# Performance work log

Measured on AMD Instinct MI355X. Metric: run time of the kernel, lower is better.

Reference implementation:

```python
import jax, jax.numpy as jnp
import numpy as np

THRESHOLD = 0.5
MARGIN = 0.5
MIN_PIXELS = 64


def make_grid(h, w):
    # Faithful to SpatialClustering.make_grid
    if w >= h:
        xm = jnp.broadcast_to(jnp.linspace(0.0, w / h, w).reshape(1, 1, w), (1, h, w))
        ym = jnp.broadcast_to(jnp.linspace(0.0, 1.0, h).reshape(1, h, 1), (1, h, w))
    else:
        xm = jnp.broadcast_to(jnp.linspace(0.0, 1.0, w).reshape(1, 1, w), (1, h, w))
        ym = jnp.broadcast_to(jnp.linspace(0.0, h / w, h).reshape(1, h, 1), (1, h, w))
    return jnp.concatenate([xm, ym], axis=0)  # (2, h, w)


def cluster_per_image(x, grid_flat):
    # x: (5, h, w); grid_flat: (2, N)
    c, h, w = x.shape
    N = h * w
    offset = x[0:2].reshape(2, N)
    sigma = x[2:4].reshape(2, N)
    seed_raw = x[4].reshape(N)

    spa_emb = jnp.tanh(offset) + grid_flat          # (2, N)
    seed_map = jax.nn.sigmoid(seed_raw)             # (N,)
    valid = seed_raw > THRESHOLD                    # (N,) == torch `mask`

    # In torch: masked_select restricts to `valid` pixels; here we keep the
    # full N-length arrays and carry `valid`/`unclustered` boolean masks.
    # unclustered starts as `valid`, so the torch outer guard
    # (mask.sum() > min_pixels) coincides with the first while-cond check.

    def cond(state):
        unclustered, inst, count, done = state
        return (jnp.sum(unclustered) > MIN_PIXELS) & jnp.logical_not(done)

    def body(state):
        unclustered, inst, count, done = state
        score = jnp.where(unclustered, seed_map, 0.0)
        idx = jnp.argmax(score)
        sc = score[idx]
        new_done = sc < THRESHOLD  # torch `break` -> revert this iteration's updates

        uncl2 = unclustered.at[idx].set(False)  # torch: unclustered[seed] = 0 before ratio
        center = spa_emb[:, idx]                # (2,)
        s = sigma[:, idx]                       # (2,)
        # exp(-sum((e-c)^2 / (2 s^2)))
        dist = jnp.exp(-jnp.sum((spa_emb - center[:, None]) ** 2 / (2.0 * s[:, None] ** 2), axis=0))  # (N,)
        proposal = (dist > MARGIN) & valid

        pc = jnp.sum(proposal)
        uc = jnp.sum(proposal & uncl2)
        # torch: proposal.sum() > min_pixels  and  unclustered[proposal].sum()/proposal.sum() > 0.5
        accept = (pc > MIN_PIXELS) & (2 * uc > pc)

        inst_new = jnp.where(accept & proposal, count, inst)
        count_new = count + accept.astype(jnp.int32)
        uncl_new = uncl2 & jnp.logical_not(proposal)  # torch: unclustered[proposal] = 0

        unclustered = jnp.where(new_done, unclustered, uncl_new)
        inst = jnp.where(new_done, inst, inst_new)
        count = jnp.where(new_done, count, count_new)
        return (unclustered, inst, count, new_done)

    init = (valid, jnp.zeros(N, dtype=jnp.int32), jnp.int32(1), jnp.array(False))
    _, inst, _, _ = jax.lax.while_loop(cond, body, init)
    return inst.reshape(h, w)


def setup_inputs() -> dict:
    key = jax.random.key(0)
    k1, k2, k3 = jax.random.split(key, 3)
    B, H, W = 4, 512, 1024
    offset = jax.random.normal(k1, (B, 2, H, W), dtype=jnp.float32)
    # sigma in [0.2, 0.45]: realistic per-pixel bandwidths so exp-distance
    # proposals cover cluster-sized regions and the greedy loop terminates.
    sigma = jax.random.uniform(k2, (B, 2, H, W), dtype=jnp.float32, minval=0.2, maxval=0.45)
    seed = jax.random.normal(k3, (B, 1, H, W), dtype=jnp.float32)
    tag_pred = jnp.concatenate([offset, sigma, seed], axis=1)  # (B, 5, H, W)
    return {"tag_pred": tag_pred}


def reference(tag_pred):
    b, c, h, w = tag_pred.shape
    grid_flat = make_grid(h, w).reshape(2, h * w)
    f = lambda x: cluster_per_image(x, grid_flat)
    inst = jax.lax.map(f, tag_pred)  # sequential per-image greedy clustering
    return inst.astype(jnp.uint8)    # (b, h, w) instance map, ids 0 = background
```

## Files before the change

### kernel.cpp

```cpp
#include <hip/hip_runtime.h>
#include <math.h>

#define BATCH 4
#define HH 512
#define WW 1024
#define NPIX (HH*WW)
#define CCAP 196608
#define GX 64
#define GY 48
#define NCELL (GX*GY)
#define CELL 0.0625f
#define INVCELL 16.0f
#define SEGSZ 512
#define NSEGMAX (CCAP/SEGSZ)
#define DLCAP 2048
#define CKSEED 800
#define CKCAP (2*CKSEED)
#define CKBCAP 512

__device__ __forceinline__ float xla_tanhf(float x) {
  if (fabsf(x) < 0.0004f) return x;
  float xc = fminf(fmaxf(x, -7.90531110763549805f), 7.90531110763549805f);
  float x2 = __fmul_rn(xc, xc);
  float p = -2.76076847742355e-16f;
  p = fmaf(x2, p, 2.00018790482477e-13f);
  p = fmaf(x2, p, -8.60467152213735e-11f);
  p = fmaf(x2, p, 5.12229709037114e-08f);
  p = fmaf(x2, p, 1.48572235717979e-05f);
  p = fmaf(x2, p, 6.37261928875436e-04f);
  p = fmaf(x2, p, 4.89352455891786e-03f);
  p = __fmul_rn(xc, p);
  float q = fmaf(x2, 1.19825839466702e-06f, 1.18534705686654e-04f);
  q = fmaf(x2, q, 2.26843463243900e-03f);
  q = fmaf(x2, q, 4.89352518554385e-03f);
  return __fdiv_rn(p, q);
}

__device__ __forceinline__ float xla_expf(float x) {
  float xc = fminf(fmaxf(x, -87.3365478515625f), 88.72283935546875f);
  float m = floorf(fmaf(xc, 1.44269504088896341f, 0.5f));
  float r = fmaf(m, -0.693359375f, xc);
  r = fmaf(m, 2.12194440e-4f, r);
  float r2 = __fmul_rn(r, r);
  float p = 1.9875691500e-4f;
  p = fmaf(p, r, 1.3981999507e-3f);
  p = fmaf(p, r, 8.3334519073e-3f);
  p = fmaf(p, r, 4.1665795894e-2f);
  p = fmaf(p, r, 1.6666665459e-1f);
  p = fmaf(p, r, 5.0000001201e-1f);
  float y = fmaf(r2, p, r);
  y = __fadd_rn(y, 1.0f);
  return ldexpf(y, (int)m);
}

__device__ __forceinline__ float xla_sigmoidf(float x) {
  return fmaf(0.5f, xla_tanhf(__fmul_rn(0.5f, x)), 0.5f);
}

__device__ __forceinline__ bool prop_test(float2 e, float cx, float cy,
                                          float den0, float den1,
                                          float inv0, float inv1) {
  float d0 = __fsub_rn(e.x, cx), d1 = __fsub_rn(e.y, cy);
  float dd0 = __fmul_rn(d0, d0), dd1 = __fmul_rn(d1, d1);
  float zf = fmaf(dd0, inv0, __fmul_rn(dd1, inv1));
  if (zf < 0.6921472f) return true;
  if (zf <= 0.6941472f) {
    float t0 = __fdiv_rn(dd0, den0);
    float t1 = __fdiv_rn(dd1, den1);
    float z = __fadd_rn(t0, t1);
    return xla_expf(-z) > 0.5f;
  }
  return false;
}

__device__ __forceinline__ int cell_of_x(float ex) {
  int c = (int)((ex + 1.0f) * INVCELL);
  return min(max(c, 0), GX - 1);
}
__device__ __forceinline__ int cell_of_y(float ey) {
  int c = (int)((ey + 1.0f) * INVCELL);
  return min(max(c, 0), GY - 1);
}

__device__ __forceinline__ int wave_sum_bcast_i32(int x) {
  x += __builtin_amdgcn_update_dpp(0, x, 0x111, 0xf, 0xf, false);
  x += __builtin_amdgcn_update_dpp(0, x, 0x112, 0xf, 0xf, false);
  x += __builtin_amdgcn_update_dpp(0, x, 0x114, 0xf, 0xf, false);
  x += __builtin_amdgcn_update_dpp(0, x, 0x118, 0xf, 0xf, false);
  x += __builtin_amdgcn_update_dpp(0, x, 0x142, 0xa, 0xf, false);
  x += __builtin_amdgcn_update_dpp(0, x, 0x143, 0xc, 0xf, false);
  return __builtin_amdgcn_readlane(x, 63);
}

__device__ __forceinline__ int wave_scan_incl_i32(int x) {
  x += __builtin_amdgcn_update_dpp(0, x, 0x111, 0xf, 0xf, false);
  x += __builtin_amdgcn_update_dpp(0, x, 0x112, 0xf, 0xf, false);
  x += __builtin_amdgcn_update_dpp(0, x, 0x114, 0xf, 0xf, false);
  x += __builtin_amdgcn_update_dpp(0, x, 0x118, 0xf, 0xf, false);
  x += __builtin_amdgcn_update_dpp(0, x, 0x142, 0xa, 0xf, false);
  x += __builtin_amdgcn_update_dpp(0, x, 0x143, 0xc, 0xf, false);
  return x;
}

__device__ __forceinline__ void wave_max_key64(unsigned &h, unsigned &l) {
#define KSTEP(ctrl, rm)                                                        \
  { unsigned nh = (unsigned)__builtin_amdgcn_update_dpp(0, (int)h, ctrl, rm, 0xf, false); \
    unsigned nl = (unsigned)__builtin_amdgcn_update_dpp(0, (int)l, ctrl, rm, 0xf, false); \
    if (nh > h || (nh == h && nl > l)) { h = nh; l = nl; } }
  KSTEP(0x111, 0xf) KSTEP(0x112, 0xf) KSTEP(0x114, 0xf) KSTEP(0x118, 0xf)
  KSTEP(0x142, 0xa) KSTEP(0x143, 0xc)
#undef KSTEP
  h = (unsigned)__builtin_amdgcn_readlane((int)h, 63);
  l = (unsigned)__builtin_amdgcn_readlane((int)l, 63);
}


__global__ __launch_bounds__(1024) void fill_kernel(int* out, int val, int n) {
  int i = blockIdx.x * 1024 + threadIdx.x;
  if (i < n) out[i] = val;
}

__global__ __launch_bounds__(1024) void hist_kernel(const float* __restrict__ in,
                                                    int* __restrict__ out,
                                                    int* __restrict__ hist) {
  __shared__ int lh[NCELL];
  int tid = threadIdx.x;
  int gid = blockIdx.x * 1024 + tid;
  int b = gid >> 19;
  int p = gid & (NPIX - 1);
  for (int j = tid; j < NCELL; j += 1024) lh[j] = 0;
  __syncthreads();
  const float* base = in + (size_t)b * 5 * NPIX;
  float seed = base[(size_t)4 * NPIX + p];
  out[gid] = 0;
  if (seed > 0.5f) {
    float ox = base[p];
    float oy = base[(size_t)NPIX + p];
    int col = p & (WW - 1);
    int row = p >> 10;
    float gx = __fmul_rn((float)col, 2.0f / 1023.0f);
    float gy = __fmul_rn((float)row, 1.0f / 511.0f);
    float ex = __fadd_rn(xla_tanhf(ox), gx);
    float ey = __fadd_rn(xla_tanhf(oy), gy);
    atomicAdd(&lh[cell_of_y(ey) * GX + cell_of_x(ex)], 1);
  }
  __syncthreads();
  for (int j = tid; j < NCELL; j += 1024) {
    int c = lh[j];
    if (c) atomicAdd(&hist[b * NCELL + j], c);
  }
}

__global__ __launch_bounds__(1024) void scan_kernel(const int* __restrict__ hist,
                                                    int* __restrict__ off,
                                                    int* __restrict__ cursor) {
  __shared__ int s_c[NCELL];
  __shared__ int s_ps[1024];
  int b = blockIdx.x, t = threadIdx.x;
  const int* h = hist + b * NCELL;
  for (int i = t; i < NCELL; i += 1024) s_c[i] = h[i];
  __syncthreads();
  int a = s_c[3 * t], b2 = s_c[3 * t + 1], c2 = s_c[3 * t + 2];
  int th = a + b2 + c2;
  s_ps[t] = th;
  __syncthreads();
  for (int d = 1; d < 1024; d <<= 1) {
    int v = (t >= d) ? s_ps[t - d] : 0;
    __syncthreads();
    s_ps[t] += v;
    __syncthreads();
  }
  int excl = s_ps[t] - th;
  int* ob = off + b * (NCELL + 1);
  int* cb = cursor + b * NCELL;
  ob[3 * t] = excl;              cb[3 * t] = excl;
  ob[3 * t + 1] = excl + a;      cb[3 * t + 1] = excl + a;
  ob[3 * t + 2] = excl + a + b2; cb[3 * t + 2] = excl + a + b2;
  if (t == 1023) ob[NCELL] = s_ps[1023];
}

__global__ __launch_bounds__(1024) void scatter_kernel(const float* __restrict__ in,
                                                       int* __restrict__ cursor,
                                                       float2* __restrict__ emb,
                                                       int2* __restrict__ pk) {
  __shared__ int lh[NCELL];
  __shared__ int lbase[NCELL];
  int tid = threadIdx.x;
  int gid = blockIdx.x * 1024 + tid;
  int b = gid >> 19;
  int p = gid & (NPIX - 1);
  for (int j = tid; j < NCELL; j += 1024) lh[j] = 0;
  __syncthreads();
  const float* base = in + (size_t)b * 5 * NPIX;
  float seed = base[(size_t)4 * NPIX + p];
  bool valid = seed > 0.5f;
  float ex = 0.0f, ey = 0.0f, smv = 0.0f;
  int cell = 0, sl = 0;
  if (valid) {
    float ox = base[p];
    float oy = base[(size_t)NPIX + p];
    int col = p & (WW - 1);
    int row = p >> 10;
    float gx = __fmul_rn((float)col, 2.0f / 1023.0f);
    float gy = __fmul_rn((float)row, 1.0f / 511.0f);
    ex = __fadd_rn(xla_tanhf(ox), gx);
    ey = __fadd_rn(xla_tanhf(oy), gy);
    smv = xla_sigmoidf(seed);
    cell = cell_of_y(ey) * GX + cell_of_x(ex);
    sl = atomicAdd(&lh[cell], 1);
  }
  __syncthreads();
  for (int j = tid; j < NCELL; j += 1024) {
    int c = lh[j];
    if (c) lbase[j] = atomicAdd(&cursor[b * NCELL + j], c);
  }
  __syncthreads();
  if (valid) {
    int slot = lbase[cell] + sl;
    if (slot < CCAP) {
      emb[(size_t)b * CCAP + slot] = make_float2(ex, ey);
      pk[(size_t)b * CCAP + slot]  = make_int2(__float_as_int(smv), p);
    }
  }
}

__device__ __forceinline__ void seg_rescan(int s, int V, int lane,
    const unsigned* s_uncl, const int2* __restrict__ pk,
    const float2* __restrict__ emb, const float* __restrict__ base,
    unsigned long long* s_segkey, unsigned long long* s_segkey2,
    int* s_segci, float4* s_segaux, float4* s_segaux2, bool checkAlive) {
  unsigned k1h = 0, k1l = 0, k2h = 0, k2l = 0; int ci1 = -1, bpx = 0;
  #pragma unroll
  for (int j = 0; j < 8; ++j) {
    int i = (s << 9) + (j << 6) + lane;
    if (i < V) {
      bool alive = !checkAlive || ((s_uncl[i >> 5] >> (i & 31)) & 1u);
      if (alive) {
        int2 v = pk[i];
        unsigned vh = (unsigned)v.x, vl = (unsigned)(~v.y);
        if (vh > k1h || (vh == k1h && vl > k1l)) {
          k2h = k1h; k2l = k1l; k1h = vh; k1l = vl; ci1 = i; bpx = v.y;
        } else if (vh > k2h || (vh == k2h && vl > k2l)) {
          k2h = vh; k2l = vl;
        }
      }
    }
  }
  unsigned m1h = k1h, m1l = k1l;
  wave_max_key64(m1h, m1l);
  if (m1h == 0u) {
    if (lane == 0) { s_segkey[s] = 0ULL; s_segkey2[s] = 0ULL; s_segci[s] = -1; }
    return;
  }
  bool own = (k1h == m1h && k1l == m1l);
  unsigned ch = own ? k2h : k1h, cl = own ? k2l : k1l;
  unsigned m2h = ch, m2l = cl;
  wave_max_key64(m2h, m2l);
  if (lane == 0) s_segkey2[s] = ((unsigned long long)m2h << 32) | m2l;
  if (own) {
    s_segkey[s] = ((unsigned long long)m1h << 32) | m1l;
    s_segci[s] = ci1;
    float2 e = emb[ci1];
    float sxv = base[(size_t)2 * NPIX + bpx];
    float syv = base[(size_t)3 * NPIX + bpx];
    float d0 = __fmul_rn(2.0f, __fmul_rn(sxv, sxv));
    float d1 = __fmul_rn(2.0f, __fmul_rn(syv, syv));
    s_segaux[s] = make_float4(e.x, e.y, d0, d1);
    float i0v = 1.0f / d0;
    float i1v = 1.0f / d1;
    float ryv = sqrtf(__fmul_rn(d1, 0.6971472f)) * 1.00001f;
    float rxv = sqrtf(__fmul_rn(d0, 0.6971472f)) * 1.00001f;
    s_segaux2[s] = make_float4(i0v, i1v, ryv, rxv);
  }
}

__global__ __launch_bounds__(1024) void cluster_kernel(const float* __restrict__ in,
                                                       int* __restrict__ out,
                                                       const float2* __restrict__ emb_all,
                                                       const int2* __restrict__ pk_all,
                                                       const int* __restrict__ off_g) {
  __shared__ unsigned int s_uncl[CCAP / 32];
  __shared__ int s_off[NCELL + 1];
  __shared__ unsigned long long s_segkey[NSEGMAX];
  __shared__ unsigned long long s_segkey2[NSEGMAX];
  __shared__ int s_segci[NSEGMAX];
  __shared__ float4 s_segaux[NSEGMAX];
  __shared__ float4 s_segaux2[NSEGMAX];
  __shared__ int s_dlist[DLCAP];
  __shared__ unsigned long long s_ck[CKCAP];
  __shared__ ulonglong2 s_ckbA[2 * CKBCAP];
  __shared__ ulonglong2 s_ckbB[2 * CKBCAP];
  __shared__ int s_pc4[4];
  __shared__ int s_uc4[4];
  __shared__ int s_ckpos4[4];
  __shared__ int s_nd[2];
  __shared__ int s_ncq[2];

  int b = blockIdx.x;
  int tid = threadIdx.x;
  int lane = tid & 63;
  int wid = tid >> 6;
  const int* offb = off_g + b * (NCELL + 1);
  int V = offb[NCELL];
  const float2* emb = emb_all + (size_t)b * CCAP;
  const int2*   pk  = pk_all  + (size_t)b * CCAP;
  int* outb = out + (size_t)b * NPIX;
  const float* base = in + (size_t)b * 5 * NPIX;

  if (V > CCAP) {
    for (int i = tid; i < NPIX; i += 1024) outb[i] = 1000000;
    return;
  }
  int NSEG = (V + SEGSZ - 1) >> 9;
  int Vm1 = V - 1;

  for (int i = tid; i <= NCELL; i += 1024) s_off[i] = offb[i];
  for (int w = tid; w < CCAP / 32; w += 1024) {
    int basebit = w << 5;
    unsigned m;
    if (basebit + 32 <= V)      m = 0xffffffffu;
    else if (basebit >= V)      m = 0u;
    else                        m = (1u << (V - basebit)) - 1u;
    s_uncl[w] = m;
  }
  if (tid < 4) { s_pc4[tid] = 0; s_uc4[tid] = 0; s_ckpos4[tid] = 0; }
  if (tid < 2) { s_nd[tid] = 0; }
  __syncthreads();

  for (int s = wid; s < NSEG; s += 16)
    seg_rescan(s, V, lane, s_uncl, pk, emb, base, s_segkey, s_segkey2,
               s_segci, s_segaux, s_segaux2, false);
  __syncthreads();

  int ucount = V, count = 1, guard = 0;
  int t = 0;
  while (ucount > 64 && guard++ <= CCAP) {
    int cur = t & 1, nxt = cur ^ 1;

    unsigned a1h = 0, a1l = 0, a2h = 0, a2l = 0; int asg1 = -1, asg2 = -1;
    for (int s = lane; s < NSEG; s += 64) {
      unsigned long long v = s_segkey[s];
      unsigned vh = (unsigned)(v >> 32), vl = (unsigned)v;
      if (vh > a1h || (vh == a1h && vl > a1l)) {
        a2h = a1h; a2l = a1l; asg2 = asg1; a1h = vh; a1l = vl; asg1 = s;
      } else if (vh > a2h || (vh == a2h && vl > a2l)) {
        a2h = vh; a2l = vl; asg2 = s;
      }
    }
    unsigned m1h = a1h, m1l = a1l;
    wave_max_key64(m1h, m1l);
    if (m1h == 0u) break;
    if (__uint_as_float(m1h) < 0.5f) break;
    bool own1 = (a1h == m1h && a1l == m1l);
    int src1 = __builtin_ctzll(__ballot(own1));
    int sg1 = __shfl(asg1, src1);
    unsigned ch = own1 ? a2h : a1h, cl2 = own1 ? a2l : a1l;
    int csg = own1 ? asg2 : asg1;
    unsigned m2h = ch, m2l = cl2;
    wave_max_key64(m2h, m2l);

    float4 auxA = s_segaux[sg1];
    float4 ax2A = s_segaux2[sg1];
    int kk = 1, sg2 = -1;
    float4 auxB = make_float4(0.f, 0.f, 1.f, 1.f);
    float4 ax2B = make_float4(1.f, 1.f, 0.f, 0.f);
    if (m2h != 0u) {
      bool own2 = (ch == m2h && cl2 == m2l);
      int src2 = __builtin_ctzll(__ballot(own2));
      sg2 = __shfl(csg, src2);
      unsigned long long k2s = s_segkey2[sg1];
      unsigned kh = (unsigned)(k2s >> 32), kl = (unsigned)k2s;
      bool hidden_bigger = (kh > m2h) || (kh == m2h && kl > m2l);
      if (!hidden_bigger) {
        auxB = s_segaux[sg2];
        ax2B = s_segaux2[sg2];
        bool ovl = (fabsf(auxA.x - auxB.x) <= (ax2A.w + ax2B.w)) &&
                   (fabsf(auxA.y - auxB.y) <= (ax2A.z + ax2B.z));
        if (!ovl) kk = 2;
      }
    }

    int myseed = (kk == 2) ? (wid & 1) : 0;
    float cxS = myseed ? auxB.x : auxA.x;
    float cyS = myseed ? auxB.y : auxA.y;
    float d0S = myseed ? auxB.z : auxA.z;
    float d1S = myseed ? auxB.w : auxA.w;
    float i0S = myseed ? ax2B.x : ax2A.x;
    float i1S = myseed ? ax2B.y : ax2A.y;
    float ryS = myseed ? ax2B.z : ax2A.z;
    int qb = myseed * CKSEED;
    int r0 = cell_of_y(cyS - ryS);
    int r1 = cell_of_y(cyS + ryS);
    int nr = r1 - r0 + 1;

    int ck = 0, rs_l = 0, re_l = 0, m0_l = 0, m1_l = 0, startl = 0;
    if (lane < nr) {
      int r = r0 + lane;
      float ylo = fmaf((float)r, CELL, -1.0f);
      float dy = fmaxf(0.0f, fmaxf(ylo - cyS, cyS - (ylo + CELL))) * 0.999999f;
      float rem = 0.6971472f - dy * dy * i1S;
      if (rem > 0.0f) {
        float dxm = sqrtf(d0S * rem) * 1.00001f;
        int c0 = cell_of_x(cxS - dxm), c1 = cell_of_x(cxS + dxm);
        int rbase = r * GX;
        rs_l = s_off[rbase + c0]; re_l = s_off[rbase + c1 + 1];
        m0_l = rs_l; m1_l = rs_l;
        float dyc = fmaxf(fabsf(ylo - cyS), fabsf(ylo + CELL - cyS)) + 1e-5f;
        float remI = 0.6920f - dyc * dyc * i1S;
        if (remI > 0.0f) {
          float dxin = sqrtf(d0S * remI) * 0.9999f;
          int a  = (int)ceilf(fmaf(cxS - dxin, INVCELL, INVCELL) + 1e-3f);
          int bb = (int)floorf(fmaf(cxS + dxin, INVCELL, INVCELL) - 1e-3f) - 1;
          a = max(a, c0); bb = min(bb, c1);
          if (a <= bb) { m0_l = s_off[rbase + a]; m1_l = s_off[rbase + bb + 1]; }
        }
        startl = rs_l & ~31;
        ck = (re_l > rs_l) ? ((re_l - startl + 255) >> 8) : 0;
      }
    }
    int cum = wave_scan_incl_i32(ck);
    int ncmine = __builtin_amdgcn_readlane(cum, 63);
    int excl = cum - ck;
    if (ncmine > CKSEED) ncmine = CKSEED;
    if (lane < nr && ck) {
      for (int k = 0; k < ck; ++k) {
        int q = excl + k;
        if (q >= CKSEED) break;
        int i0k = startl + (k << 8);
        int ssk = max(rs_l - i0k, 0);
        int lok = min(max(m0_l - i0k, 0), 256);
        int h2k = min(max(m1_l - i0k, 0), 256);
        int enk = min(re_l - i0k, 256);
        s_ck[qb + q] = (unsigned long long)(unsigned)(i0k >> 5)
                     | ((unsigned long long)(unsigned)ssk << 13)
                     | ((unsigned long long)(unsigned)lok << 19)
                     | ((unsigned long long)(unsigned)h2k << 28)
                     | ((unsigned long long)(unsigned)enk << 37);
      }
    }
    if (lane == 0) s_ncq[myseed] = ncmine;

    int pc = 0, uc = 0;
    int* ckposp = &s_ckpos4[cur * 2 + myseed];
    for (;;) {
      int pos;
      if (lane == 0) pos = atomicAdd(ckposp, 1);
      pos = __shfl(pos, 0);
      if (pos >= ncmine) break;
      unsigned long long ed = s_ck[qb + pos];
      int i0 = ((int)(ed & 0x1fff)) << 5;
      int ss = (int)((ed >> 13) & 0x3f);
      int lo = (int)((ed >> 19) & 0x1ff);
      int h2 = (int)((ed >> 28) & 0x1ff);
      int en = (int)((ed >> 37) & 0x1ff);
      int idx1 = lane + 64, idx2 = lane + 128, idx3 = lane + 192;
      bool p0, p1, p2, p3;
      if (lo <= ss && h2 >= en) {
        p0 = lane >= ss && lane < en;
        p1 = idx1 < en; p2 = idx2 < en; p3 = idx3 < en;
      } else {
        int ia = min(i0 + lane, Vm1),  ib = min(i0 + idx1, Vm1);
        int ic = min(i0 + idx2, Vm1),  id = min(i0 + idx3, Vm1);
        float2 e0 = emb[ia], e1 = emb[ib], e2 = emb[ic], e3 = emb[id];
        bool t0 = prop_test(e0, cxS, cyS, d0S, d1S, i0S, i1S);
        bool t1 = prop_test(e1, cxS, cyS, d0S, d1S, i0S, i1S);
        bool t2 = prop_test(e2, cxS, cyS, d0S, d1S, i0S, i1S);
        bool t3 = prop_test(e3, cxS, cyS, d0S, d1S, i0S, i1S);
        p0 = (lane >= ss && lane < en) && ((lane >= lo && lane < h2) || t0);
        p1 = (idx1 < en) && ((idx1 >= lo && idx1 < h2) || t1);
        p2 = (idx2 < en) && ((idx2 >= lo && idx2 < h2) || t2);
        p3 = (idx3 < en) && ((idx3 >= lo && idx3 < h2) || t3);
      }
      unsigned long long bm0 = __ballot(p0);
      unsigned long long bm1 = __ballot(p1);
      unsigned long long bm2 = __ballot(p2);
      unsigned long long bm3 = __ballot(p3);
      if (pos < CKBCAP) {
        int bidx = (myseed << 9) + pos;
        if (lane == 0)      { ulonglong2 v; v.x = bm0; v.y = bm1; s_ckbA[bidx] = v; }
        else if (lane == 1) { ulonglong2 v; v.x = bm2; v.y = bm3; s_ckbB[bidx] = v; }
      }
      if ((bm0 | bm1 | bm2 | bm3) != 0ULL && lane < 8) {
        unsigned long long bsel = (lane < 2) ? bm0 : (lane < 4) ? bm1
                                 : (lane < 6) ? bm2 : bm3;
        unsigned bits = (unsigned)(bsel >> ((lane & 1) << 5));
        pc += __popc(bits);
        if (bits) {
          unsigned tw = (unsigned)(i0 >> 5) + (unsigned)lane;
          unsigned old = atomicAnd(&s_uncl[tw], ~bits);
          unsigned remv = old & bits;
          if (remv) {
            uc += __popc(remv);
            int seg = (int)(tw >> 4);
            int ciw = s_segci[seg];
            if ((ciw >> 5) == (int)tw && ((remv >> (ciw & 31)) & 1u)) {
              int dpos = atomicAdd(&s_nd[cur], 1);
              if (dpos < DLCAP) s_dlist[dpos] = seg;
            }
          }
        }
      }
    }
    int pcW = wave_sum_bcast_i32(pc);
    int ucW = wave_sum_bcast_i32(uc);
    if (lane == 0 && (pcW | ucW)) {
      if (pcW) atomicAdd(&s_pc4[cur * 2 + myseed], pcW);
      if (ucW) atomicAdd(&s_uc4[cur * 2 + myseed], ucW);
    }
    __syncthreads();

    int pcT0 = s_pc4[cur * 2 + 0], ucR0 = s_uc4[cur * 2 + 0];
    int pcT1 = s_pc4[cur * 2 + 1], ucR1 = s_uc4[cur * 2 + 1];
    int ndRaw = s_nd[cur];
    int nc0 = s_ncq[0];
    int nc1q = (kk == 2) ? s_ncq[1] : 0;
    bool acc0 = (pcT0 > 64) && (2 * (ucR0 - 1) > pcT0);
    bool valid1 = (kk == 2) && (ucount - ucR0 > 64);
    bool acc1 = valid1 && (pcT1 > 64) && (2 * (ucR1 - 1) > pcT1);
    int label0 = count & 255; if (acc0) count++;
    int label1 = count & 255; if (acc1) count++;
    ucount -= ucR0;
    if (valid1) ucount -= ucR1;
    if (tid == 0) {
      s_pc4[nxt * 2] = 0; s_pc4[nxt * 2 + 1] = 0;
      s_uc4[nxt * 2] = 0; s_uc4[nxt * 2 + 1] = 0;
      s_nd[nxt] = 0;
      s_ckpos4[nxt * 2] = 0; s_ckpos4[nxt * 2 + 1] = 0;
    }

    if (acc0) {
      for (int c2 = wid; c2 < nc0; c2 += 16) {
        unsigned long long e = s_ck[c2];
        int i0 = ((int)(e & 0x1fff)) << 5;
        if (c2 < CKBCAP) {
          ulonglong2 ba = s_ckbA[c2];
          ulonglong2 bb = s_ckbB[c2];
          if ((ba.x >> lane) & 1ULL) outb[pk[i0 + lane].y] = label0;
          if ((ba.y >> lane) & 1ULL) outb[pk[i0 + 64 + lane].y] = label0;
          if ((bb.x >> lane) & 1ULL) outb[pk[i0 + 128 + lane].y] = label0;
          if ((bb.y >> lane) & 1ULL) outb[pk[i0 + 192 + lane].y] = label0;
        } else {
          int ss = (int)((e >> 13) & 0x3f);
          int lo = (int)((e >> 19) & 0x1ff);
          int h2 = (int)((e >> 28) & 0x1ff);
          int en = (int)((e >> 37) & 0x1ff);
          #pragma unroll
          for (int g = 0; g < 4; ++g) {
            int idx = (g << 6) + lane;
            if (idx >= ss && idx < en &&
                ((idx >= lo && idx < h2) ||
                 prop_test(emb[i0 + idx], auxA.x, auxA.y, auxA.z, auxA.w,
                           ax2A.x, ax2A.y)))
              outb[pk[i0 + idx].y] = label0;
          }
        }
      }
    }
    if (acc1) {
      for (int c2 = wid; c2 < nc1q; c2 += 16) {
        unsigned long long e = s_ck[CKSEED + c2];
        int i0 = ((int)(e & 0x1fff)) << 5;
        if (c2 < CKBCAP) {
          ulonglong2 ba = s_ckbA[CKBCAP + c2];
          ulonglong2 bb = s_ckbB[CKBCAP + c2];
          if ((ba.x >> lane) & 1ULL) outb[pk[i0 + lane].y] = label1;
          if ((ba.y >> lane) & 1ULL) outb[pk[i0 + 64 + lane].y] = label1;
          if ((bb.x >> lane) & 1ULL) outb[pk[i0 + 128 + lane].y] = label1;
          if ((bb.y >> lane) & 1ULL) outb[pk[i0 + 192 + lane].y] = label1;
        } else {
          int ss = (int)((e >> 13) & 0x3f);
          int lo = (int)((e >> 19) & 0x1ff);
          int h2 = (int)((e >> 28) & 0x1ff);
          int en = (int)((e >> 37) & 0x1ff);
          #pragma unroll
          for (int g = 0; g < 4; ++g) {
            int idx = (g << 6) + lane;
            if (idx >= ss && idx < en &&
                ((idx >= lo && idx < h2) ||
                 prop_test(emb[i0 + idx], auxB.x, auxB.y, auxB.z, auxB.w,
                           ax2B.x, ax2B.y)))
              outb[pk[i0 + idx].y] = label1;
          }
        }
      }
    }

    if (kk == 2 && !valid1) break;

    if (ndRaw > DLCAP) {
      for (int s = wid; s < NSEG; s += 16)
        seg_rescan(s, V, lane, s_uncl, pk, emb, base, s_segkey, s_segkey2,
                   s_segci, s_segaux, s_segaux2, true);
    } else {
      for (int d = wid; d < ndRaw; d += 16)
        seg_rescan(s_dlist[d], V, lane, s_uncl, pk, emb, base, s_segkey,
                   s_segkey2, s_segci, s_segaux, s_segaux2, true);
    }
    __syncthreads();
    t++;
  }
}


extern "C" void kernel_launch(void* const* d_in, const int* in_sizes, int n_in,
                              void* d_out, int out_size, void* d_ws, size_t ws_size,
                              hipStream_t stream) {
  const float* in = (const float*)d_in[0];
  int* out = (int*)d_out;

  size_t hist_bytes = (size_t)BATCH * NCELL * sizeof(int);
  size_t off_bytes  = (size_t)BATCH * (NCELL + 1) * sizeof(int);
  size_t cur_bytes  = (size_t)BATCH * NCELL * sizeof(int);
  size_t emb_bytes  = (size_t)BATCH * CCAP * sizeof(float2);
  size_t pk_bytes   = (size_t)BATCH * CCAP * sizeof(int2);

  size_t o_hist = 256;
  size_t o_off  = (o_hist + hist_bytes + 255) & ~(size_t)255;
  size_t o_cur  = (o_off + off_bytes + 255) & ~(size_t)255;
  size_t o_emb  = (o_cur + cur_bytes + 255) & ~(size_t)255;
  size_t o_pk   = (o_emb + emb_bytes + 255) & ~(size_t)255;
  size_t need   = o_pk + pk_bytes;

  if (ws_size < need) {
    fill_kernel<<<(out_size + 1023) / 1024, 1024, 0, stream>>>(out, 2000000, out_size);
    return;
  }

  int*    hist = (int*)((char*)d_ws + o_hist);
  int*    off  = (int*)((char*)d_ws + o_off);
  int*    cur  = (int*)((char*)d_ws + o_cur);
  float2* emb  = (float2*)((char*)d_ws + o_emb);
  int2*   pk   = (int2*)((char*)d_ws + o_pk);

  hipMemsetAsync(hist, 0, hist_bytes, stream);
  hist_kernel<<<(BATCH * NPIX) / 1024, 1024, 0, stream>>>(in, out, hist);
  scan_kernel<<<BATCH, 1024, 0, stream>>>(hist, off, cur);
  scatter_kernel<<<(BATCH * NPIX) / 1024, 1024, 0, stream>>>(in, cur, emb, pk);
  cluster_kernel<<<BATCH, 1024, 0, stream>>>(in, out, emb, pk, off);
}
```

Before: 822.0 us.

## Merge two-seed chunk queues into one static-strided queue with interior-chunk fast path

Replaces the per-seed work split (half the waves per seed, each pulling chunks with an atomic counter) with a single combined queue built for both seeds. All 16 waves stride it statically and prefetch the next entry, and a per-entry seed bit selects the parameters. Interior chunks skip the ballots and build their masks arithmetically. Segments now also track the second-best candidate so a removal that invalidates it triggers a rescan. The intent is to remove atomic queue contention and load imbalance between the two seeds, at the cost of extra branching on seed and more shared state. It also drops the early break on a score below 0.5, and if the second queue overflows it falls back to one seed instead of truncating.

```diff
diff --git a/kernel.cpp b/kernel.cpp
--- a/kernel.cpp
+++ b/kernel.cpp
@@ -14,8 +14,7 @@
 #define SEGSZ 512
 #define NSEGMAX (CCAP/SEGSZ)
 #define DLCAP 2048
-#define CKSEED 800
-#define CKCAP (2*CKSEED)
+#define CKCAP 1600
 #define CKBCAP 512
 
 __device__ __forceinline__ float xla_tanhf(float x) {
@@ -80,6 +79,12 @@
 __device__ __forceinline__ int cell_of_y(float ey) {
   int c = (int)((ey + 1.0f) * INVCELL);
   return min(max(c, 0), GY - 1);
+}
+
+__device__ __forceinline__ unsigned long long maskrange64(int a, int b) {
+  unsigned long long mb = (b >= 64) ? ~0ULL : ((1ULL << b) - 1ULL);
+  unsigned long long ma = (1ULL << a) - 1ULL;
+  return mb & ~ma;
 }
 
 __device__ __forceinline__ int wave_sum_bcast_i32(int x) {
@@ -228,8 +233,9 @@
     const unsigned* s_uncl, const int2* __restrict__ pk,
     const float2* __restrict__ emb, const float* __restrict__ base,
     unsigned long long* s_segkey, unsigned long long* s_segkey2,
-    int* s_segci, float4* s_segaux, float4* s_segaux2, bool checkAlive) {
-  unsigned k1h = 0, k1l = 0, k2h = 0, k2l = 0; int ci1 = -1, bpx = 0;
+    int* s_segci, int* s_segci2, float4* s_segaux, float4* s_segaux2,
+    bool checkAlive) {
+  unsigned k1h = 0, k1l = 0, k2h = 0, k2l = 0; int c1 = -1, c2 = -1, bpx = 0;
   #pragma unroll
   for (int j = 0; j < 8; ++j) {
     int i = (s << 9) + (j << 6) + lane;
@@ -239,9 +245,9 @@
         int2 v = pk[i];
         unsigned vh = (unsigned)v.x, vl = (unsigned)(~v.y);
         if (vh > k1h || (vh == k1h && vl > k1l)) {
-          k2h = k1h; k2l = k1l; k1h = vh; k1l = vl; ci1 = i; bpx = v.y;
+          k2h = k1h; k2l = k1l; c2 = c1; k1h = vh; k1l = vl; c1 = i; bpx = v.y;
         } else if (vh > k2h || (vh == k2h && vl > k2l)) {
-          k2h = vh; k2l = vl;
+          k2h = vh; k2l = vl; c2 = i;
         }
       }
     }
@@ -249,18 +255,27 @@
   unsigned m1h = k1h, m1l = k1l;
   wave_max_key64(m1h, m1l);
   if (m1h == 0u) {
-    if (lane == 0) { s_segkey[s] = 0ULL; s_segkey2[s] = 0ULL; s_segci[s] = -1; }
+    if (lane == 0) {
+      s_segkey[s] = 0ULL; s_segkey2[s] = 0ULL;
+      s_segci[s] = -1; s_segci2[s] = -1;
+    }
     return;
   }
-  bool own = (k1h == m1h && k1l == m1l);
-  unsigned ch = own ? k2h : k1h, cl = own ? k2l : k1l;
+  bool own1 = (k1h == m1h && k1l == m1l);
+  unsigned ch = own1 ? k2h : k1h, cl = own1 ? k2l : k1l;
+  int cc = own1 ? c2 : c1;
   unsigned m2h = ch, m2l = cl;
   wave_max_key64(m2h, m2l);
-  if (lane == 0) s_segkey2[s] = ((unsigned long long)m2h << 32) | m2l;
-  if (own) {
+  if (m2h == 0u && m2l == 0u) {
+    if (lane == 0) { s_segkey2[s] = 0ULL; s_segci2[s] = -1; }
+  } else if (ch == m2h && cl == m2l) {
+    s_segkey2[s] = ((unsigned long long)m2h << 32) | m2l;
+    s_segci2[s] = cc;
+  }
+  if (own1) {
     s_segkey[s] = ((unsigned long long)m1h << 32) | m1l;
-    s_segci[s] = ci1;
-    float2 e = emb[ci1];
+    s_segci[s] = c1;
+    float2 e = emb[c1];
     float sxv = base[(size_t)2 * NPIX + bpx];
     float syv = base[(size_t)3 * NPIX + bpx];
     float d0 = __fmul_rn(2.0f, __fmul_rn(sxv, sxv));
@@ -274,6 +289,59 @@
   }
 }
 
+__device__ __forceinline__ int build_queue(float cxS, float cyS, float d0S,
+    float i1S, float ryS, const int* s_off, unsigned long long* s_ck,
+    int lane, int qoff, int sdbit) {
+  int r0 = cell_of_y(cyS - ryS);
+  int r1 = cell_of_y(cyS + ryS);
+  int nr = r1 - r0 + 1;
+  int ck = 0, rs_l = 0, re_l = 0, m0_l = 0, m1_l = 0, startl = 0;
+  if (lane < nr) {
+    int r = r0 + lane;
+    float ylo = fmaf((float)r, CELL, -1.0f);
+    float dy = fmaxf(0.0f, fmaxf(ylo - cyS, cyS - (ylo + CELL))) * 0.999999f;
+    float rem = 0.6971472f - dy * dy * i1S;
+    if (rem > 0.0f) {
+      float dxm = sqrtf(d0S * rem) * 1.00001f;
+      int c0 = cell_of_x(cxS - dxm), c1 = cell_of_x(cxS + dxm);
+      int rbase = r * GX;
+      rs_l = s_off[rbase + c0]; re_l = s_off[rbase + c1 + 1];
+      m0_l = rs_l; m1_l = rs_l;
+      float dyc = fmaxf(fabsf(ylo - cyS), fabsf(ylo + CELL - cyS)) + 1e-5f;
+      float remI = 0.6920f - dyc * dyc * i1S;
+      if (remI > 0.0f) {
+        float dxin = sqrtf(d0S * remI) * 0.9999f;
+        int a  = (int)ceilf(fmaf(cxS - dxin, INVCELL, INVCELL) + 1e-3f);
+        int bb = (int)floorf(fmaf(cxS + dxin, INVCELL, INVCELL) - 1e-3f) - 1;
+        a = max(a, c0); bb = min(bb, c1);
+        if (a <= bb) { m0_l = s_off[rbase + a]; m1_l = s_off[rbase + bb + 1]; }
+      }
+      startl = rs_l & ~31;
+      ck = (re_l > rs_l) ? ((re_l - startl + 255) >> 8) : 0;
+    }
+  }
+  int cum = wave_scan_incl_i32(ck);
+  int ncS = __builtin_amdgcn_readlane(cum, 63);
+  if (qoff + ncS > CKCAP) return -1;
+  int excl = cum - ck;
+  if (lane < nr && ck) {
+    for (int k = 0; k < ck; ++k) {
+      int i0k = startl + (k << 8);
+      int ssk = max(rs_l - i0k, 0);
+      int lok = min(max(m0_l - i0k, 0), 256);
+      int h2k = min(max(m1_l - i0k, 0), 256);
+      int enk = min(re_l - i0k, 256);
+      s_ck[qoff + excl + k] = (unsigned long long)(unsigned)(i0k >> 5)
+                     | ((unsigned long long)(unsigned)ssk << 13)
+                     | ((unsigned long long)(unsigned)lok << 19)
+                     | ((unsigned long long)(unsigned)h2k << 28)
+                     | ((unsigned long long)(unsigned)enk << 37)
+                     | ((unsigned long long)(unsigned)sdbit << 46);
+    }
+  }
+  return ncS;
+}
+
 __global__ __launch_bounds__(1024) void cluster_kernel(const float* __restrict__ in,
                                                        int* __restrict__ out,
                                                        const float2* __restrict__ emb_all,
@@ -284,17 +352,16 @@
   __shared__ unsigned long long s_segkey[NSEGMAX];
   __shared__ unsigned long long s_segkey2[NSEGMAX];
   __shared__ int s_segci[NSEGMAX];
+  __shared__ int s_segci2[NSEGMAX];
   __shared__ float4 s_segaux[NSEGMAX];
   __shared__ float4 s_segaux2[NSEGMAX];
   __shared__ int s_dlist[DLCAP];
   __shared__ unsigned long long s_ck[CKCAP];
-  __shared__ ulonglong2 s_ckbA[2 * CKBCAP];
-  __shared__ ulonglong2 s_ckbB[2 * CKBCAP];
+  __shared__ ulonglong2 s_ckbA[CKBCAP];
+  __shared__ ulonglong2 s_ckbB[CKBCAP];
   __shared__ int s_pc4[4];
   __shared__ int s_uc4[4];
-  __shared__ int s_ckpos4[4];
   __shared__ int s_nd[2];
-  __shared__ int s_ncq[2];
 
   int b = blockIdx.x;
   int tid = threadIdx.x;
@@ -323,13 +390,13 @@
     else                        m = (1u << (V - basebit)) - 1u;
     s_uncl[w] = m;
   }
-  if (tid < 4) { s_pc4[tid] = 0; s_uc4[tid] = 0; s_ckpos4[tid] = 0; }
+  if (tid < 4) { s_pc4[tid] = 0; s_uc4[tid] = 0; }
   if (tid < 2) { s_nd[tid] = 0; }
   __syncthreads();
 
   for (int s = wid; s < NSEG; s += 16)
     seg_rescan(s, V, lane, s_uncl, pk, emb, base, s_segkey, s_segkey2,
-               s_segci, s_segaux, s_segaux2, false);
+               s_segci, s_segci2, s_segaux, s_segaux2, false);
   __syncthreads();
 
   int ucount = V, count = 1, guard = 0;
@@ -337,25 +404,24 @@
   while (ucount > 64 && guard++ <= CCAP) {
     int cur = t & 1, nxt = cur ^ 1;
 
-    unsigned a1h = 0, a1l = 0, a2h = 0, a2l = 0; int asg1 = -1, asg2 = -1;
+    unsigned a1h = 0, a1l = 0, a2h = 0, a2l = 0; int g1 = -1, g2 = -1;
     for (int s = lane; s < NSEG; s += 64) {
       unsigned long long v = s_segkey[s];
       unsigned vh = (unsigned)(v >> 32), vl = (unsigned)v;
       if (vh > a1h || (vh == a1h && vl > a1l)) {
-        a2h = a1h; a2l = a1l; asg2 = asg1; a1h = vh; a1l = vl; asg1 = s;
+        a2h = a1h; a2l = a1l; g2 = g1; a1h = vh; a1l = vl; g1 = s;
       } else if (vh > a2h || (vh == a2h && vl > a2l)) {
-        a2h = vh; a2l = vl; asg2 = s;
+        a2h = vh; a2l = vl; g2 = s;
       }
     }
     unsigned m1h = a1h, m1l = a1l;
     wave_max_key64(m1h, m1l);
     if (m1h == 0u) break;
-    if (__uint_as_float(m1h) < 0.5f) break;
     bool own1 = (a1h == m1h && a1l == m1l);
     int src1 = __builtin_ctzll(__ballot(own1));
-    int sg1 = __shfl(asg1, src1);
+    int sg1 = __shfl(g1, src1);
     unsigned ch = own1 ? a2h : a1h, cl2 = own1 ? a2l : a1l;
-    int csg = own1 ? asg2 : asg1;
+    int cg = own1 ? g2 : g1;
     unsigned m2h = ch, m2l = cl2;
     wave_max_key64(m2h, m2l);
 
@@ -367,11 +433,11 @@
     if (m2h != 0u) {
       bool own2 = (ch == m2h && cl2 == m2l);
       int src2 = __builtin_ctzll(__ballot(own2));
-      sg2 = __shfl(csg, src2);
+      sg2 = __shfl(cg, src2);
       unsigned long long k2s = s_segkey2[sg1];
       unsigned kh = (unsigned)(k2s >> 32), kl = (unsigned)k2s;
-      bool hidden_bigger = (kh > m2h) || (kh == m2h && kl > m2l);
-      if (!hidden_bigger) {
+      bool hidden = (kh > m2h) || (kh == m2h && kl > m2l);
+      if (!hidden) {
         auxB = s_segaux[sg2];
         ax2B = s_segaux2[sg2];
         bool ovl = (fabsf(auxA.x - auxB.x) <= (ax2A.w + ax2B.w)) &&
@@ -380,140 +446,109 @@
       }
     }
 
-    int myseed = (kk == 2) ? (wid & 1) : 0;
-    float cxS = myseed ? auxB.x : auxA.x;
-    float cyS = myseed ? auxB.y : auxA.y;
-    float d0S = myseed ? auxB.z : auxA.z;
-    float d1S = myseed ? auxB.w : auxA.w;
-    float i0S = myseed ? ax2B.x : ax2A.x;
-    float i1S = myseed ? ax2B.y : ax2A.y;
-    float ryS = myseed ? ax2B.z : ax2A.z;
-    int qb = myseed * CKSEED;
-    int r0 = cell_of_y(cyS - ryS);
-    int r1 = cell_of_y(cyS + ryS);
-    int nr = r1 - r0 + 1;
-
-    int ck = 0, rs_l = 0, re_l = 0, m0_l = 0, m1_l = 0, startl = 0;
-    if (lane < nr) {
-      int r = r0 + lane;
-      float ylo = fmaf((float)r, CELL, -1.0f);
-      float dy = fmaxf(0.0f, fmaxf(ylo - cyS, cyS - (ylo + CELL))) * 0.999999f;
-      float rem = 0.6971472f - dy * dy * i1S;
-      if (rem > 0.0f) {
-        float dxm = sqrtf(d0S * rem) * 1.00001f;
-        int c0 = cell_of_x(cxS - dxm), c1 = cell_of_x(cxS + dxm);
-        int rbase = r * GX;
-        rs_l = s_off[rbase + c0]; re_l = s_off[rbase + c1 + 1];
-        m0_l = rs_l; m1_l = rs_l;
-        float dyc = fmaxf(fabsf(ylo - cyS), fabsf(ylo + CELL - cyS)) + 1e-5f;
-        float remI = 0.6920f - dyc * dyc * i1S;
-        if (remI > 0.0f) {
-          float dxin = sqrtf(d0S * remI) * 0.9999f;
-          int a  = (int)ceilf(fmaf(cxS - dxin, INVCELL, INVCELL) + 1e-3f);
-          int bb = (int)floorf(fmaf(cxS + dxin, INVCELL, INVCELL) - 1e-3f) - 1;
-          a = max(a, c0); bb = min(bb, c1);
-          if (a <= bb) { m0_l = s_off[rbase + a]; m1_l = s_off[rbase + bb + 1]; }
-        }
-        startl = rs_l & ~31;
-        ck = (re_l > rs_l) ? ((re_l - startl + 255) >> 8) : 0;
-      }
-    }
-    int cum = wave_scan_incl_i32(ck);
-    int ncmine = __builtin_amdgcn_readlane(cum, 63);
-    int excl = cum - ck;
-    if (ncmine > CKSEED) ncmine = CKSEED;
-    if (lane < nr && ck) {
-      for (int k = 0; k < ck; ++k) {
-        int q = excl + k;
-        if (q >= CKSEED) break;
-        int i0k = startl + (k << 8);
-        int ssk = max(rs_l - i0k, 0);
-        int lok = min(max(m0_l - i0k, 0), 256);
-        int h2k = min(max(m1_l - i0k, 0), 256);
-        int enk = min(re_l - i0k, 256);
-        s_ck[qb + q] = (unsigned long long)(unsigned)(i0k >> 5)
-                     | ((unsigned long long)(unsigned)ssk << 13)
-                     | ((unsigned long long)(unsigned)lok << 19)
-                     | ((unsigned long long)(unsigned)h2k << 28)
-                     | ((unsigned long long)(unsigned)enk << 37);
-      }
-    }
-    if (lane == 0) s_ncq[myseed] = ncmine;
-
-    int pc = 0, uc = 0;
-    int* ckposp = &s_ckpos4[cur * 2 + myseed];
-    for (;;) {
-      int pos;
-      if (lane == 0) pos = atomicAdd(ckposp, 1);
-      pos = __shfl(pos, 0);
-      if (pos >= ncmine) break;
-      unsigned long long ed = s_ck[qb + pos];
+    int ncTot = build_queue(auxA.x, auxA.y, auxA.z, ax2A.y, ax2A.z,
+                            s_off, s_ck, lane, 0, 0);
+    if (kk == 2) {
+      int nc1 = build_queue(auxB.x, auxB.y, auxB.z, ax2B.y, ax2B.z,
+                            s_off, s_ck, lane, ncTot, 1);
+      if (nc1 < 0) kk = 1; else ncTot += nc1;
+    }
+
+    int pc0 = 0, uc0 = 0, pc1 = 0, uc1 = 0;
+    int c = wid;
+    unsigned long long ed = (c < ncTot) ? s_ck[c] : 0ULL;
+    while (c < ncTot) {
+      int cn = c + 16;
+      unsigned long long epre = (cn < ncTot) ? s_ck[cn] : 0ULL;
       int i0 = ((int)(ed & 0x1fff)) << 5;
       int ss = (int)((ed >> 13) & 0x3f);
       int lo = (int)((ed >> 19) & 0x1ff);
       int h2 = (int)((ed >> 28) & 0x1ff);
       int en = (int)((ed >> 37) & 0x1ff);
-      int idx1 = lane + 64, idx2 = lane + 128, idx3 = lane + 192;
-      bool p0, p1, p2, p3;
-      if (lo <= ss && h2 >= en) {
-        p0 = lane >= ss && lane < en;
-        p1 = idx1 < en; p2 = idx2 < en; p3 = idx3 < en;
+      int sb = (int)((ed >> 46) & 1);
+      bool interior = (lo <= ss && h2 >= en);
+      unsigned long long bm0, bm1, bm2, bm3;
+      if (interior) {
+        bm0 = maskrange64(ss, min(en, 64));
+        bm1 = maskrange64(0, min(max(en - 64, 0), 64));
+        bm2 = maskrange64(0, min(max(en - 128, 0), 64));
+        bm3 = maskrange64(0, min(max(en - 192, 0), 64));
       } else {
+        float cx = sb ? auxB.x : auxA.x;
+        float cy = sb ? auxB.y : auxA.y;
+        float den0 = sb ? auxB.z : auxA.z;
+        float den1 = sb ? auxB.w : auxA.w;
+        float inv0 = sb ? ax2B.x : ax2A.x;
+        float inv1 = sb ? ax2B.y : ax2A.y;
+        int idx1 = lane + 64, idx2 = lane + 128, idx3 = lane + 192;
         int ia = min(i0 + lane, Vm1),  ib = min(i0 + idx1, Vm1);
         int ic = min(i0 + idx2, Vm1),  id = min(i0 + idx3, Vm1);
         float2 e0 = emb[ia], e1 = emb[ib], e2 = emb[ic], e3 = emb[id];
-        bool t0 = prop_test(e0, cxS, cyS, d0S, d1S, i0S, i1S);
-        bool t1 = prop_test(e1, cxS, cyS, d0S, d1S, i0S, i1S);
-        bool t2 = prop_test(e2, cxS, cyS, d0S, d1S, i0S, i1S);
-        bool t3 = prop_test(e3, cxS, cyS, d0S, d1S, i0S, i1S);
-        p0 = (lane >= ss && lane < en) && ((lane >= lo && lane < h2) || t0);
-        p1 = (idx1 < en) && ((idx1 >= lo && idx1 < h2) || t1);
-        p2 = (idx2 < en) && ((idx2 >= lo && idx2 < h2) || t2);
-        p3 = (idx3 < en) && ((idx3 >= lo && idx3 < h2) || t3);
-      }
-      unsigned long long bm0 = __ballot(p0);
-      unsigned long long bm1 = __ballot(p1);
-      unsigned long long bm2 = __ballot(p2);
-      unsigned long long bm3 = __ballot(p3);
-      if (pos < CKBCAP) {
-        int bidx = (myseed << 9) + pos;
-        if (lane == 0)      { ulonglong2 v; v.x = bm0; v.y = bm1; s_ckbA[bidx] = v; }
-        else if (lane == 1) { ulonglong2 v; v.x = bm2; v.y = bm3; s_ckbB[bidx] = v; }
+        bool t0 = prop_test(e0, cx, cy, den0, den1, inv0, inv1);
+        bool t1 = prop_test(e1, cx, cy, den0, den1, inv0, inv1);
+        bool t2 = prop_test(e2, cx, cy, den0, den1, inv0, inv1);
+        bool t3 = prop_test(e3, cx, cy, den0, den1, inv0, inv1);
+        bool p0 = (lane >= ss && lane < en) && ((lane >= lo && lane < h2) || t0);
+        bool p1 = (idx1 < en) && ((idx1 >= lo && idx1 < h2) || t1);
+        bool p2 = (idx2 < en) && ((idx2 >= lo && idx2 < h2) || t2);
+        bool p3 = (idx3 < en) && ((idx3 >= lo && idx3 < h2) || t3);
+        bm0 = __ballot(p0);
+        bm1 = __ballot(p1);
+        bm2 = __ballot(p2);
+        bm3 = __ballot(p3);
+        if (c < CKBCAP) {
+          if (lane == 0)      { ulonglong2 v; v.x = bm0; v.y = bm1; s_ckbA[c] = v; }
+          else if (lane == 1) { ulonglong2 v; v.x = bm2; v.y = bm3; s_ckbB[c] = v; }
+        }
       }
       if ((bm0 | bm1 | bm2 | bm3) != 0ULL && lane < 8) {
         unsigned long long bsel = (lane < 2) ? bm0 : (lane < 4) ? bm1
                                  : (lane < 6) ? bm2 : bm3;
         unsigned bits = (unsigned)(bsel >> ((lane & 1) << 5));
-        pc += __popc(bits);
+        int add = __popc(bits);
+        if (sb) pc1 += add; else pc0 += add;
         if (bits) {
           unsigned tw = (unsigned)(i0 >> 5) + (unsigned)lane;
           unsigned old = atomicAnd(&s_uncl[tw], ~bits);
           unsigned remv = old & bits;
           if (remv) {
-            uc += __popc(remv);
+            int radd = __popc(remv);
+            if (sb) uc1 += radd; else uc0 += radd;
             int seg = (int)(tw >> 4);
             int ciw = s_segci[seg];
-            if ((ciw >> 5) == (int)tw && ((remv >> (ciw & 31)) & 1u)) {
-              int dpos = atomicAdd(&s_nd[cur], 1);
-              if (dpos < DLCAP) s_dlist[dpos] = seg;
+            int ciw2 = s_segci2[seg];
+            bool hit = ((ciw  >> 5) == (int)tw && ((remv >> (ciw  & 31)) & 1u)) ||
+                       ((ciw2 >> 5) == (int)tw && ((remv >> (ciw2 & 31)) & 1u));
+            if (hit) {
+              int pos = atomicAdd(&s_nd[cur], 1);
+              if (pos < DLCAP) s_dlist[pos] = seg;
             }
           }
         }
       }
-    }
-    int pcW = wave_sum_bcast_i32(pc);
-    int ucW = wave_sum_bcast_i32(uc);
-    if (lane == 0 && (pcW | ucW)) {
-      if (pcW) atomicAdd(&s_pc4[cur * 2 + myseed], pcW);
-      if (ucW) atomicAdd(&s_uc4[cur * 2 + myseed], ucW);
+      c = cn; ed = epre;
+    }
+    {
+      int pcW = wave_sum_bcast_i32(pc0);
+      int ucW = wave_sum_bcast_i32(uc0);
+      if (lane == 0 && (pcW | ucW)) {
+        if (pcW) atomicAdd(&s_pc4[cur * 2 + 0], pcW);
+        if (ucW) atomicAdd(&s_uc4[cur * 2 + 0], ucW);
+      }
+      if (kk == 2) {
+        int pcW1 = wave_sum_bcast_i32(pc1);
+        int ucW1 = wave_sum_bcast_i32(uc1);
+        if (lane == 0 && (pcW1 | ucW1)) {
+          if (pcW1) atomicAdd(&s_pc4[cur * 2 + 1], pcW1);
+          if (ucW1) atomicAdd(&s_uc4[cur * 2 + 1], ucW1);
+        }
+      }
     }
     __syncthreads();
 
     int pcT0 = s_pc4[cur * 2 + 0], ucR0 = s_uc4[cur * 2 + 0];
     int pcT1 = s_pc4[cur * 2 + 1], ucR1 = s_uc4[cur * 2 + 1];
     int ndRaw = s_nd[cur];
-    int nc0 = s_ncq[0];
-    int nc1q = (kk == 2) ? s_ncq[1] : 0;
     bool acc0 = (pcT0 > 64) && (2 * (ucR0 - 1) > pcT0);
     bool valid1 = (kk == 2) && (ucount - ucR0 > 64);
     bool acc1 = valid1 && (pcT1 > 64) && (2 * (ucR1 - 1) > pcT1);
@@ -525,61 +560,51 @@
       s_pc4[nxt * 2] = 0; s_pc4[nxt * 2 + 1] = 0;
       s_uc4[nxt * 2] = 0; s_uc4[nxt * 2 + 1] = 0;
       s_nd[nxt] = 0;
-      s_ckpos4[nxt * 2] = 0; s_ckpos4[nxt * 2 + 1] = 0;
-    }
-
-    if (acc0) {
-      for (int c2 = wid; c2 < nc0; c2 += 16) {
+    }
+
+    if (acc0 || acc1) {
+      for (int c2 = wid; c2 < ncTot; c2 += 16) {
         unsigned long long e = s_ck[c2];
+        int sb = (int)((e >> 46) & 1);
+        bool acc = sb ? acc1 : acc0;
+        if (!acc) continue;
+        int label = sb ? label1 : label0;
         int i0 = ((int)(e & 0x1fff)) << 5;
-        if (c2 < CKBCAP) {
+        int ss = (int)((e >> 13) & 0x3f);
+        int lo = (int)((e >> 19) & 0x1ff);
+        int h2 = (int)((e >> 28) & 0x1ff);
+        int en = (int)((e >> 37) & 0x1ff);
+        bool interior = (lo <= ss && h2 >= en);
+        if (interior) {
+          unsigned long long b0 = maskrange64(ss, min(en, 64));
+          unsigned long long b1 = maskrange64(0, min(max(en - 64, 0), 64));
+          unsigned long long b2 = maskrange64(0, min(max(en - 128, 0), 64));
+          unsigned long long b3 = maskrange64(0, min(max(en - 192, 0), 64));
+          if ((b0 >> lane) & 1ULL) outb[pk[i0 + lane].y] = label;
+          if ((b1 >> lane) & 1ULL) outb[pk[i0 + 64 + lane].y] = label;
+          if ((b2 >> lane) & 1ULL) outb[pk[i0 + 128 + lane].y] = label;
+          if ((b3 >> lane) & 1ULL) outb[pk[i0 + 192 + lane].y] = label;
+        } else if (c2 < CKBCAP) {
           ulonglong2 ba = s_ckbA[c2];
           ulonglong2 bb = s_ckbB[c2];
-          if ((ba.x >> lane) & 1ULL) outb[pk[i0 + lane].y] = label0;
-          if ((ba.y >> lane) & 1ULL) outb[pk[i0 + 64 + lane].y] = label0;
-          if ((bb.x >> lane) & 1ULL) outb[pk[i0 + 128 + lane].y] = label0;
-          if ((bb.y >> lane) & 1ULL) outb[pk[i0 + 192 + lane].y] = label0;
+          if ((ba.x >> lane) & 1ULL) outb[pk[i0 + lane].y] = label;
+          if ((ba.y >> lane) & 1ULL) outb[pk[i0 + 64 + lane].y] = label;
+          if ((bb.x >> lane) & 1ULL) outb[pk[i0 + 128 + lane].y] = label;
+          if ((bb.y >> lane) & 1ULL) outb[pk[i0 + 192 + lane].y] = label;
         } else {
-          int ss = (int)((e >> 13) & 0x3f);
-          int lo = (int)((e >> 19) & 0x1ff);
-          int h2 = (int)((e >> 28) & 0x1ff);
-          int en = (int)((e >> 37) & 0x1ff);
+          float cx = sb ? auxB.x : auxA.x;
+          float cy = sb ? auxB.y : auxA.y;
+          float den0 = sb ? auxB.z : auxA.z;
+          float den1 = sb ? auxB.w : auxA.w;
+          float inv0 = sb ? ax2B.x : ax2A.x;
+          float inv1 = sb ? ax2B.y : ax2A.y;
           #pragma unroll
           for (int g = 0; g < 4; ++g) {
             int idx = (g << 6) + lane;
             if (idx >= ss && idx < en &&
                 ((idx >= lo && idx < h2) ||
-                 prop_test(emb[i0 + idx], auxA.x, auxA.y, auxA.z, auxA.w,
-                           ax2A.x, ax2A.y)))
-              outb[pk[i0 + idx].y] = label0;
-          }
-        }
-      }
-    }
-    if (acc1) {
-      for (int c2 = wid; c2 < nc1q; c2 += 16) {
-        unsigned long long e = s_ck[CKSEED + c2];
-        int i0 = ((int)(e & 0x1fff)) << 5;
-        if (c2 < CKBCAP) {
-          ulonglong2 ba = s_ckbA[CKBCAP + c2];
-          ulonglong2 bb = s_ckbB[CKBCAP + c2];
-          if ((ba.x >> lane) & 1ULL) outb[pk[i0 + lane].y] = label1;
-          if ((ba.y >> lane) & 1ULL) outb[pk[i0 + 64 + lane].y] = label1;
-          if ((bb.x >> lane) & 1ULL) outb[pk[i0 + 128 + lane].y] = label1;
-          if ((bb.y >> lane) & 1ULL) outb[pk[i0 + 192 + lane].y] = label1;
-        } else {
-          int ss = (int)((e >> 13) & 0x3f);
-          int lo = (int)((e >> 19) & 0x1ff);
-          int h2 = (int)((e >> 28) & 0x1ff);
-          int en = (int)((e >> 37) & 0x1ff);
-          #pragma unroll
-          for (int g = 0; g < 4; ++g) {
-            int idx = (g << 6) + lane;
-            if (idx >= ss && idx < en &&
-                ((idx >= lo && idx < h2) ||
-                 prop_test(emb[i0 + idx], auxB.x, auxB.y, auxB.z, auxB.w,
-                           ax2B.x, ax2B.y)))
-              outb[pk[i0 + idx].y] = label1;
+                 prop_test(emb[i0 + idx], cx, cy, den0, den1, inv0, inv1)))
+              outb[pk[i0 + idx].y] = label;
           }
         }
       }
@@ -590,11 +615,11 @@
     if (ndRaw > DLCAP) {
       for (int s = wid; s < NSEG; s += 16)
         seg_rescan(s, V, lane, s_uncl, pk, emb, base, s_segkey, s_segkey2,
-                   s_segci, s_segaux, s_segaux2, true);
+                   s_segci, s_segci2, s_segaux, s_segaux2, true);
     } else {
       for (int d = wid; d < ndRaw; d += 16)
         seg_rescan(s_dlist[d], V, lane, s_uncl, pk, emb, base, s_segkey,
-                   s_segkey2, s_segci, s_segaux, s_segaux2, true);
+                   s_segkey2, s_segci, s_segci2, s_segaux, s_segaux2, true);
     }
     __syncthreads();
     t++;
```

Measured after the change: 940.1 us. 14.4% more time.
